# Optimization experiments

Hardware: AMD Instinct MI355X
Metric: run time of the kernel (lower is better)

## Reference

```python
import jax, jax.numpy as jnp
import numpy as np

H = 256      # hidden_dim
NH = 8       # num_heads
D = H // NH  # per-head dim
NEG = -(2.0**32) + 1.0
EPS = 1e-5


def setup_inputs() -> dict:
    key = jax.random.key(0)
    ks = jax.random.split(key, 12)
    N, Tq, Tk = 2, 2048, 2048
    s = 1.0 / np.sqrt(H)
    return {
        "Q": jax.random.normal(ks[0], (N, Tq, H), jnp.float32),
        "K": jax.random.normal(ks[1], (N, Tk, H), jnp.float32),
        "V": jax.random.normal(ks[2], (N, Tk, H), jnp.float32),
        "Wq": jax.random.normal(ks[3], (H, H), jnp.float32) * s,
        "bq": jnp.zeros((H,), jnp.float32),
        "Wk": jax.random.normal(ks[4], (H, H), jnp.float32) * s,
        "bk": jnp.zeros((H,), jnp.float32),
        "Wv": jax.random.normal(ks[5], (H, H), jnp.float32) * s,
        "bv": jnp.zeros((H,), jnp.float32),
        "gamma": jnp.ones((H,), jnp.float32),
        "beta": jnp.zeros((H,), jnp.float32),
    }


def _split_heads(x):
    # [N,T,H] -> [h,N,T,D]  (matches torch split(dim=2)+cat(dim=0): head-major)
    N, T, _ = x.shape
    return x.reshape(N, T, NH, D).transpose(2, 0, 1, 3)


def reference(Q, K, V, Wq, bq, Wk, bk, Wv, bv, gamma, beta):
    N, Tq, _ = Q.shape
    Tk = K.shape[1]
    Ql = jax.nn.relu(Q @ Wq + bq)
    Kl = jax.nn.relu(K @ Wk + bk)
    Vl = jax.nn.relu(V @ Wv + bv)
    Qh, Kh, Vh = _split_heads(Ql), _split_heads(Kl), _split_heads(Vl)

    scores = jnp.einsum("hnqd,hnkd->hnqk", Qh, Kh) / jnp.sqrt(jnp.float32(D))
    key_mask = jnp.sign(jnp.abs(K).sum(-1))    # [N,Tk]
    scores = jnp.where(key_mask[None, :, None, :] == 0, NEG, scores)
    attn = jax.nn.softmax(scores / 0.01, axis=-1)
    query_mask = jnp.sign(jnp.abs(Q).sum(-1))  # [N,Tq]
    attn = attn * query_mask[None, :, :, None]  # dropout p=0 -> identity

    ctx = jnp.einsum("hnqk,hnkd->hnqd", attn[..., :-1], Vh[:, :, :-1, :])
    out = ctx.transpose(1, 2, 0, 3).reshape(N, Tq, H)

    mu = out.mean(-1, keepdims=True)
    var = ((out - mu) ** 2).mean(-1, keepdims=True)
    out = (out - mu) / jnp.sqrt(var + EPS) * gamma + beta

    weight = attn.transpose(1, 2, 0, 3).reshape(N, Tq, NH * Tk).mean(-1)
    return out, weight
```

## Files before the change

### kernel.cpp

```cpp
#include <hip/hip_runtime.h>
#include <math.h>

#define H_DIM 256
#define NHEAD 8
#define DHEAD 32
#define NB 2
#define TSEQ 2048
#define LN_EPS 1e-5f

#define QK2_SCALE 25.503486f
#define SPLIT 4
#define TILES_PER (TSEQ / 64 / SPLIT)

typedef _Float16 half8 __attribute__((ext_vector_type(8)));
typedef _Float16 half4t __attribute__((ext_vector_type(4)));
typedef _Float16 half2t __attribute__((ext_vector_type(2)));
typedef float f32x4 __attribute__((ext_vector_type(4)));

__device__ __forceinline__ f32x4 mfma16(half8 a, half8 b, f32x4 c) {
  return __builtin_amdgcn_mfma_f32_16x16x32_f16(a, b, c, 0, 0, 0);
}
__device__ __forceinline__ float exp2fast(float x) {
  return __builtin_amdgcn_exp2f(x);
}
__device__ __forceinline__ half2t pkrtz(float a, float b) {
  return __builtin_bit_cast(half2t, __builtin_amdgcn_cvt_pkrtz(a, b));
}

#define GLOAD_LDS(gp, lp)                                            \
  __builtin_amdgcn_global_load_lds(                                  \
      (const __attribute__((address_space(1))) void*)(gp),           \
      (__attribute__((address_space(3))) void*)(lp), 16, 0, 0)

__global__ __launch_bounds__(256, 3) void proj_kernel(
    const float* __restrict__ Q, const float* __restrict__ K, const float* __restrict__ V,
    const float* __restrict__ Wq, const float* __restrict__ Wk, const float* __restrict__ Wv,
    const float* __restrict__ bq, const float* __restrict__ bk, const float* __restrict__ bv,
    half8* __restrict__ Gqhi, half8* __restrict__ Gqlo,
    half8* __restrict__ Gkhi, half8* __restrict__ Gklo, half8* __restrict__ Gv,
    float* __restrict__ qmask, float* __restrict__ kmask) {
  const int which = blockIdx.z;
  const float* X    = which == 0 ? Q  : which == 1 ? K  : V;
  const float* Wsel = which == 0 ? Wq : which == 1 ? Wk : Wv;
  const float* bias = which == 0 ? bq : which == 1 ? bk : bv;

  __shared__ __align__(16) float T[64 * 68];

  const int tid = threadIdx.x;
  const int w = tid >> 6, lane = tid & 63;
  const int l15 = lane & 15, quad = lane >> 4;
  const int mbase = blockIdx.y * 64;
  const int nfg   = blockIdx.x * 4;
  const int nn   = mbase >> 11;
  const int tile = blockIdx.y & 31;

  half8 ahi[8], alo[8];
  {
    const bool domask = (blockIdx.x == 0) && (which < 2);
    float sabs = 0.0f;
    const float* xrow = X + (size_t)(mbase + w * 16 + l15) * H_DIM + quad * 8;
    #pragma unroll
    for (int s = 0; s < 8; ++s) {
      float4 a0 = *(const float4*)(xrow + s * 32);
      float4 a1 = *(const float4*)(xrow + s * 32 + 4);
      float xs[8] = {a0.x, a0.y, a0.z, a0.w, a1.x, a1.y, a1.z, a1.w};
      if (domask) {
        #pragma unroll
        for (int i = 0; i < 8; ++i) sabs += fabsf(xs[i]);
      }
      #pragma unroll
      for (int i = 0; i < 8; ++i) {
        _Float16 h = (_Float16)xs[i];
        ahi[s][i] = h;
        alo[s][i] = (_Float16)(xs[i] - (float)h);
      }
    }
    if (domask) {
      sabs += __shfl_xor(sabs, 16);
      sabs += __shfl_xor(sabs, 32);
      float* dst = (which == 0) ? qmask : kmask;
      if (quad == 0) dst[mbase + w * 16 + l15] = (sabs != 0.0f) ? 1.0f : 0.0f;
    }
  }

  f32x4 acc[4];
  #pragma unroll
  for (int f = 0; f < 4; ++f) acc[f] = (f32x4){0.f, 0.f, 0.f, 0.f};

  #pragma unroll
  for (int s = 0; s < 8; ++s) {
    #pragma unroll
    for (int f = 0; f < 4; ++f) {
      const float* wp = Wsel + (size_t)(s * 32 + quad * 8) * H_DIM + (nfg + f) * 16 + l15;
      half8 BH, BL;
      #pragma unroll
      for (int jj = 0; jj < 8; ++jj) {
        float x = wp[(size_t)jj * H_DIM];
        _Float16 h = (_Float16)x;
        BH[jj] = h;
        BL[jj] = (_Float16)(x - (float)h);
      }
      acc[f] = mfma16(ahi[s], BH, acc[f]);
      acc[f] = mfma16(ahi[s], BL, acc[f]);
      acc[f] = mfma16(alo[s], BH, acc[f]);
    }
  }

  #pragma unroll
  for (int f = 0; f < 4; ++f) {
    float bj = bias[blockIdx.x * 64 + f * 16 + l15];
    #pragma unroll
    for (int r = 0; r < 4; ++r) {
      int row = w * 16 + quad * 4 + r;
      float val = fmaxf(acc[f][r] + bj, 0.0f);
      if (which == 2 && ((mbase + row) & (TSEQ - 1)) == TSEQ - 1) val = 0.0f;
      T[row * 68 + f * 16 + l15] = val;
    }
  }
  __syncthreads();

  if (which < 2) {
    const int fq = tid >> 6, lp = tid & 63;
    const int kdc = lp >> 4, krlo = lp & 15;
    const int row = fq * 16 + krlo;
    const float sc = (which == 0) ? QK2_SCALE : 1.0f;
    #pragma unroll
    for (int hs = 0; hs < 2; ++hs) {
      const float* p = &T[row * 68 + hs * 32 + kdc * 8];
      float4 a0 = *(const float4*)p;
      float4 a1 = *(const float4*)(p + 4);
      float xs[8] = {a0.x, a0.y, a0.z, a0.w, a1.x, a1.y, a1.z, a1.w};
      half8 hi, lo;
      #pragma unroll
      for (int i = 0; i < 8; ++i) {
        float x = xs[i] * sc;
        _Float16 h = (_Float16)x;
        hi[i] = h;
        lo[i] = (_Float16)(x - (float)h);
      }
      int hn = (blockIdx.x * 2 + hs) * NB + nn;
      size_t di = ((size_t)hn * 32 + tile) * 256 + tid;
      if (which == 0) { Gqhi[di] = hi; Gqlo[di] = lo; }
      else            { Gkhi[di] = hi; Gklo[di] = lo; }
    }
  } else {
    const int top = tid >> 6, mid = (tid >> 4) & 3, low = tid & 15;
    const int c = top >> 1, hh = top & 1;
    const int trow0 = (c * 4 + mid) * 8;
    #pragma unroll
    for (int hs = 0; hs < 2; ++hs) {
      const int col = hs * 32 + hh * 16 + low;
      half8 v8;
      #pragma unroll
      for (int j = 0; j < 8; ++j)
        v8[j] = (_Float16)T[(trow0 + j) * 68 + col];
      int hn = (blockIdx.x * 2 + hs) * NB + nn;
      Gv[((size_t)hn * 32 + tile) * 256 + tid] = v8;
    }
  }
}

__global__ __launch_bounds__(256, 4) void attn_kernel(
    const half8* __restrict__ Gqhi, const half8* __restrict__ Gqlo,
    const half8* __restrict__ Gkhi, const half8* __restrict__ Gklo,
    const half8* __restrict__ Gv, const float* __restrict__ kmask,
    _Float16* __restrict__ Opf, float* __restrict__ Mp, float* __restrict__ Lp) {
  __shared__ __align__(16) half8 KhB[2][256];
  __shared__ __align__(16) half8 KlB[2][256];
  __shared__ __align__(16) half8 VB[2][256];
  __shared__ __align__(16) float kmS[2][64];
  __shared__ __align__(16) _Float16 Pbuf[4][16][72];

  const int tid = threadIdx.x;
  const int w = tid >> 6, lane = tid & 63;
  const int l15 = lane & 15, quad = lane >> 4;

  const int b = blockIdx.x;
  const int g    = ((b & 7) << 1) | ((b >> 3) & 1);
  const int qt   = (b >> 4) & 15;
  const int sblk = b >> 8;
  const int n = g & 1;

  const size_t fbase = (size_t)g * 32 * 256;
  const int tile0 = sblk * TILES_PER;

  const size_t qoff = fbase + (size_t)(qt * 2) * 256 + w * 64 + lane;
  half8 qhiA = Gqhi[qoff];
  half8 qloA = Gqlo[qoff];
  half8 qhiB = Gqhi[qoff + 256];
  half8 qloB = Gqlo[qoff + 256];

  half8 amONE;
  #pragma unroll
  for (int j = 0; j < 8; ++j) amONE[j] = (l15 == 0) ? (_Float16)1.0f : (_Float16)0.0f;

  float mA = -1.0e30f, mB = -1.0e30f;
  f32x4 O0A = {0.f,0.f,0.f,0.f}, O1A = O0A, OlA = O0A;
  f32x4 O0B = O0A, O1B = O0A, OlB = O0A;

  const half8* gkh = Gkhi + fbase + (size_t)tile0 * 256;
  const half8* gkl = Gklo + fbase + (size_t)tile0 * 256;
  const half8* gvv = Gv   + fbase + (size_t)tile0 * 256;
  const float* kmg = kmask + (size_t)n * TSEQ + tile0 * 64;

  GLOAD_LDS(gkh + tid, &KhB[0][tid]);
  GLOAD_LDS(gkl + tid, &KlB[0][tid]);
  GLOAD_LDS(gvv + tid, &VB[0][tid]);
  if (tid < 16) GLOAD_LDS(kmg + tid * 4, &kmS[0][tid * 4]);
  __syncthreads();

  #pragma unroll
  for (int tt = 0; tt < TILES_PER; ++tt) {
    const int cur = tt & 1, nxt = cur ^ 1;
    if (tt < TILES_PER - 1) {
      GLOAD_LDS(gkh + (tt + 1) * 256 + tid, &KhB[nxt][tid]);
      GLOAD_LDS(gkl + (tt + 1) * 256 + tid, &KlB[nxt][tid]);
      GLOAD_LDS(gvv + (tt + 1) * 256 + tid, &VB[nxt][tid]);
      if (tid < 16) GLOAD_LDS(kmg + (tt + 1) * 64 + tid * 4, &kmS[nxt][tid * 4]);
    }

    f32x4 SA[4], SB[4];
    #pragma unroll
    for (int f = 0; f < 4; ++f) {
      half8 KH = KhB[cur][f * 64 + lane];
      half8 KL = KlB[cur][f * 64 + lane];
      f32x4 a = (f32x4){0.f, 0.f, 0.f, 0.f};
      a = mfma16(KL, qhiA, a);
      a = mfma16(KH, qloA, a);
      a = mfma16(KH, qhiA, a);
      SA[f] = a;
      f32x4 bb = (f32x4){0.f, 0.f, 0.f, 0.f};
      bb = mfma16(KL, qhiB, bb);
      bb = mfma16(KH, qloB, bb);
      bb = mfma16(KH, qhiB, bb);
      SB[f] = bb;
    }

    const half8* vbuf = (const half8*)VB[cur];
    const float* kmP = &kmS[cur][0];

#define SM_PV(S, m_q, O0, O1, Ol)                                              \
    {                                                                          \
      float t0 = fmaxf(fmaxf(S[0][0], S[0][1]), fmaxf(S[0][2], S[0][3]));      \
      float t1 = fmaxf(fmaxf(S[1][0], S[1][1]), fmaxf(S[1][2], S[1][3]));      \
      float t2 = fmaxf(fmaxf(S[2][0], S[2][1]), fmaxf(S[2][2], S[2][3]));      \
      float t3 = fmaxf(fmaxf(S[3][0], S[3][1]), fmaxf(S[3][2], S[3][3]));      \
      float mx = fmaxf(fmaxf(t0, t1), fmaxf(t2, t3));                          \
      mx = fmaxf(mx, __shfl_xor(mx, 16));                                      \
      mx = fmaxf(mx, __shfl_xor(mx, 32));                                      \
      float mnew = fmaxf(m_q, mx);                                             \
      float alpha = exp2fast(m_q - mnew);                                      \
      m_q = mnew;                                                              \
      _Pragma("unroll")                                                        \
      for (int f = 0; f < 4; ++f) {                                            \
        f32x4 kmv = *(const f32x4*)&kmP[f * 16 + quad * 4];                    \
        float p0 = exp2fast(S[f][0] - m_q) * kmv[0];                           \
        float p1 = exp2fast(S[f][1] - m_q) * kmv[1];                           \
        float p2 = exp2fast(S[f][2] - m_q) * kmv[2];                           \
        float p3 = exp2fast(S[f][3] - m_q) * kmv[3];                           \
        half2t a01 = pkrtz(p0, p1);                                            \
        half2t a23 = pkrtz(p2, p3);                                            \
        half4t pk4;                                                            \
        pk4[0] = a01[0]; pk4[1] = a01[1]; pk4[2] = a23[0]; pk4[3] = a23[1];    \
        *(half4t*)&Pbuf[w][l15][f * 16 + quad * 4] = pk4;                      \
      }                                                                        \
      _Pragma("unroll")                                                        \
      for (int r = 0; r < 4; ++r) { O0[r] *= alpha; O1[r] *= alpha; }          \
      Ol[0] *= alpha;                                                          \
      asm volatile("s_waitcnt lgkmcnt(0)" ::: "memory");                       \
      _Pragma("unroll")                                                        \
      for (int c = 0; c < 2; ++c) {                                            \
        half8 pb = *(const half8*)&Pbuf[w][l15][c * 32 + quad * 8];            \
        O0 = mfma16(vbuf[(c * 2 + 0) * 64 + lane], pb, O0);                    \
        O1 = mfma16(vbuf[(c * 2 + 1) * 64 + lane], pb, O1);                    \
        Ol = mfma16(amONE, pb, Ol);                                            \
      }                                                                        \
    }

    SM_PV(SA, mA, O0A, O1A, OlA)
    SM_PV(SB, mB, O0B, O1B, OlB)
#undef SM_PV

    __syncthreads();
  }

  {
    int qA = qt * 128 + w * 16 + l15;
    size_t rowbase = (size_t)(sblk * 16 + g) * TSEQ;
    size_t idxA = (rowbase + qA) * DHEAD;
    size_t idxB = (rowbase + qA + 64) * DHEAD;
    half4t o0A = {(_Float16)O0A[0], (_Float16)O0A[1], (_Float16)O0A[2], (_Float16)O0A[3]};
    half4t o1A = {(_Float16)O1A[0], (_Float16)O1A[1], (_Float16)O1A[2], (_Float16)O1A[3]};
    half4t o0B = {(_Float16)O0B[0], (_Float16)O0B[1], (_Float16)O0B[2], (_Float16)O0B[3]};
    half4t o1B = {(_Float16)O1B[0], (_Float16)O1B[1], (_Float16)O1B[2], (_Float16)O1B[3]};
    *(half4t*)&Opf[idxA + quad * 4]      = o0A;
    *(half4t*)&Opf[idxA + 16 + quad * 4] = o1A;
    *(half4t*)&Opf[idxB + quad * 4]      = o0B;
    *(half4t*)&Opf[idxB + 16 + quad * 4] = o1B;
    if (quad == 0) {
      Mp[rowbase + qA]      = mA;
      Lp[rowbase + qA]      = OlA[0];
      Mp[rowbase + qA + 64] = mB;
      Lp[rowbase + qA + 64] = OlB[0];
    }
  }
}

__global__ __launch_bounds__(256) void ln_kernel(
    const _Float16* __restrict__ Opf, const float* __restrict__ Mp, const float* __restrict__ Lp,
    const float* __restrict__ gamma, const float* __restrict__ beta,
    const float* __restrict__ qmask,
    float* __restrict__ out, float* __restrict__ wout) {
  const int wid = threadIdx.x >> 6, lane = threadIdx.x & 63;
  const int row = blockIdx.x * 4 + wid;
  const int n = row >> 11, q = row & (TSEQ - 1);
  const int hh = lane >> 3;
  const int hn = hh * NB + n;
  const int dbase = (lane & 7) * 4;

  float m[SPLIT], l[SPLIT];
  half4t P[SPLIT];
  #pragma unroll
  for (int i = 0; i < SPLIT; ++i) {
    size_t si = (size_t)(i * 16 + hn) * TSEQ + q;
    P[i] = *(const half4t*)&Opf[si * DHEAD + dbase];
    m[i] = Mp[si];
    l[i] = Lp[si];
  }
  float mm = m[0];
  #pragma unroll
  for (int i = 1; i < SPLIT; ++i) mm = fmaxf(mm, m[i]);
  float denom = 0.f;
  float a[SPLIT];
  #pragma unroll
  for (int i = 0; i < SPLIT; ++i) { a[i] = exp2fast(m[i] - mm); denom += l[i] * a[i]; }
  float qm = qmask[row];
  float inv = qm / denom;

  float4 x = make_float4(0.f, 0.f, 0.f, 0.f);
  #pragma unroll
  for (int i = 0; i < SPLIT; ++i) {
    x.x += (float)P[i][0] * a[i]; x.y += (float)P[i][1] * a[i];
    x.z += (float)P[i][2] * a[i]; x.w += (float)P[i][3] * a[i];
  }
  x.x *= inv; x.y *= inv; x.z *= inv; x.w *= inv;

  float s = x.x + x.y + x.z + x.w;
  #pragma unroll
  for (int off = 32; off > 0; off >>= 1) s += __shfl_xor(s, off);
  float mu = s * (1.0f / H_DIM);
  float dx0 = x.x - mu, dx1 = x.y - mu, dx2 = x.z - mu, dx3 = x.w - mu;
  float sq = dx0 * dx0 + dx1 * dx1 + dx2 * dx2 + dx3 * dx3;
  #pragma unroll
  for (int off = 32; off > 0; off >>= 1) sq += __shfl_xor(sq, off);
  float rstd = rsqrtf(sq * (1.0f / H_DIM) + LN_EPS);
  float4 g = *(const float4*)(gamma + lane * 4);
  float4 bb = *(const float4*)(beta + lane * 4);
  float4 y;
  y.x = dx0 * rstd * g.x + bb.x;
  y.y = dx1 * rstd * g.y + bb.y;
  y.z = dx2 * rstd * g.z + bb.z;
  y.w = dx3 * rstd * g.w + bb.w;
  *(float4*)(out + (size_t)row * H_DIM + lane * 4) = y;
  if (lane == 0) wout[row] = qm * (1.0f / TSEQ);
}

extern "C" void kernel_launch(void* const* d_in, const int* in_sizes, int n_in,
                              void* d_out, int out_size, void* d_ws, size_t ws_size,
                              hipStream_t stream) {
  const float* Q  = (const float*)d_in[0];
  const float* K  = (const float*)d_in[1];
  const float* V  = (const float*)d_in[2];
  const float* Wq = (const float*)d_in[3];
  const float* bq = (const float*)d_in[4];
  const float* Wk = (const float*)d_in[5];
  const float* bk = (const float*)d_in[6];
  const float* Wv = (const float*)d_in[7];
  const float* bv = (const float*)d_in[8];
  const float* gamma = (const float*)d_in[9];
  const float* beta  = (const float*)d_in[10];

  char* ws = (char*)d_ws;
  const size_t NFRAG = (size_t)16 * 32 * 256;
  _Float16* Opf = (_Float16*)ws;
  half8* Gqhi = (half8*)(ws + (size_t)SPLIT * 16 * TSEQ * DHEAD * 2);
  half8* Gqlo = Gqhi + NFRAG;
  half8* Gkhi = Gqlo + NFRAG;
  half8* Gklo = Gkhi + NFRAG;
  half8* Gv   = Gklo + NFRAG;
  float* Mp = (float*)(Gv + NFRAG);
  float* Lp = Mp + SPLIT * 16 * TSEQ;
  float* qmask = Lp + SPLIT * 16 * TSEQ;
  float* kmask = qmask + NB * TSEQ;

  float* out  = (float*)d_out;
  float* wout = out + (size_t)NB * TSEQ * H_DIM;

  hipLaunchKernelGGL(proj_kernel, dim3(H_DIM / 64, NB * TSEQ / 64, 3), dim3(256), 0, stream,
                     Q, K, V, Wq, Wk, Wv, bq, bk, bv,
                     Gqhi, Gqlo, Gkhi, Gklo, Gv, qmask, kmask);
  hipLaunchKernelGGL(attn_kernel, dim3(16 * 16 * SPLIT), dim3(256), 0, stream,
                     Gqhi, Gqlo, Gkhi, Gklo, Gv, kmask, Opf, Mp, Lp);
  hipLaunchKernelGGL(ln_kernel, dim3(NB * TSEQ / 4), dim3(256), 0, stream,
                     Opf, Mp, Lp, gamma, beta, qmask, out, wout);
}
```

Baseline: 126.6 us.

## Pre-pack split-fp16 weights once and narrow projection tiles to one head

Adds a pre-pass kernel that computes the key mask and converts Wq/Wk/Wv once into hi/lo fp16 fragments laid out in MFMA order. The projection kernel then loads these packed fragments directly instead of re-reading strided fp32 weights and re-splitting them in every block. Each block now covers one 32-wide head instead of 64 columns, which doubles the grid and halves the accumulators and shared memory, so occupancy can rise. The cost is an extra kernel launch, extra workspace, and each input row being loaded twice as often.

Result: slower. 132.9 us (+5.0%).

```diff
diff --git a/kernel.cpp b/kernel.cpp
--- a/kernel.cpp
+++ b/kernel.cpp
@@ -32,31 +32,67 @@
       (const __attribute__((address_space(1))) void*)(gp),           \
       (__attribute__((address_space(3))) void*)(lp), 16, 0, 0)
 
-__global__ __launch_bounds__(256, 3) void proj_kernel(
+__global__ __launch_bounds__(256) void pack_mask_kernel(
+    const float* __restrict__ K,
+    const float* __restrict__ Wq, const float* __restrict__ Wk, const float* __restrict__ Wv,
+    float* __restrict__ kmask,
+    half8* __restrict__ WpkHi, half8* __restrict__ WpkLo) {
+  const int tid = threadIdx.x;
+  if (blockIdx.x < 1024) {
+    const int wid = tid >> 6, lane = tid & 63;
+    int row = blockIdx.x * 4 + wid;
+    const float* src = K + (size_t)row * H_DIM;
+    float4 v = *(const float4*)(src + lane * 4);
+    float s = fabsf(v.x) + fabsf(v.y) + fabsf(v.z) + fabsf(v.w);
+    #pragma unroll
+    for (int off = 32; off > 0; off >>= 1) s += __shfl_xor(s, off);
+    if (lane == 0) kmask[row] = (s != 0.0f) ? 1.0f : 0.0f;
+    return;
+  }
+  int slot = (blockIdx.x - 1024) * 256 + tid;
+  int lane = slot & 63;
+  int fg = (slot >> 6) & 15;
+  int s  = (slot >> 10) & 7;
+  int which = slot >> 13;
+  const float* W = which == 0 ? Wq : which == 1 ? Wk : Wv;
+  int j  = fg * 16 + (lane & 15);
+  int kb = s * 32 + (lane >> 4) * 8;
+  half8 hi, lo;
+  #pragma unroll
+  for (int jj = 0; jj < 8; ++jj) {
+    float x = W[(size_t)(kb + jj) * H_DIM + j];
+    _Float16 h = (_Float16)x;
+    hi[jj] = h;
+    lo[jj] = (_Float16)(x - (float)h);
+  }
+  WpkHi[slot] = hi;
+  WpkLo[slot] = lo;
+}
+
+__global__ __launch_bounds__(256, 4) void proj_kernel(
     const float* __restrict__ Q, const float* __restrict__ K, const float* __restrict__ V,
-    const float* __restrict__ Wq, const float* __restrict__ Wk, const float* __restrict__ Wv,
     const float* __restrict__ bq, const float* __restrict__ bk, const float* __restrict__ bv,
+    const half8* __restrict__ WpkHi, const half8* __restrict__ WpkLo,
     half8* __restrict__ Gqhi, half8* __restrict__ Gqlo,
     half8* __restrict__ Gkhi, half8* __restrict__ Gklo, half8* __restrict__ Gv,
-    float* __restrict__ qmask, float* __restrict__ kmask) {
+    float* __restrict__ qmask) {
   const int which = blockIdx.z;
   const float* X    = which == 0 ? Q  : which == 1 ? K  : V;
-  const float* Wsel = which == 0 ? Wq : which == 1 ? Wk : Wv;
   const float* bias = which == 0 ? bq : which == 1 ? bk : bv;
 
-  __shared__ __align__(16) float T[64 * 68];
+  __shared__ __align__(16) float T[64 * 36];
 
   const int tid = threadIdx.x;
   const int w = tid >> 6, lane = tid & 63;
   const int l15 = lane & 15, quad = lane >> 4;
   const int mbase = blockIdx.y * 64;
-  const int nfg   = blockIdx.x * 4;
+  const int xh    = blockIdx.x;
   const int nn   = mbase >> 11;
   const int tile = blockIdx.y & 31;
 
   half8 ahi[8], alo[8];
   {
-    const bool domask = (blockIdx.x == 0) && (which < 2);
+    const bool doqm = (which == 0) && (xh == 0);
     float sabs = 0.0f;
     const float* xrow = X + (size_t)(mbase + w * 16 + l15) * H_DIM + quad * 8;
     #pragma unroll
@@ -64,7 +100,7 @@
       float4 a0 = *(const float4*)(xrow + s * 32);
       float4 a1 = *(const float4*)(xrow + s * 32 + 4);
       float xs[8] = {a0.x, a0.y, a0.z, a0.w, a1.x, a1.y, a1.z, a1.w};
-      if (domask) {
+      if (doqm) {
         #pragma unroll
         for (int i = 0; i < 8; ++i) sabs += fabsf(xs[i]);
       }
@@ -75,31 +111,25 @@
         alo[s][i] = (_Float16)(xs[i] - (float)h);
       }
     }
-    if (domask) {
+    if (doqm) {
       sabs += __shfl_xor(sabs, 16);
       sabs += __shfl_xor(sabs, 32);
-      float* dst = (which == 0) ? qmask : kmask;
-      if (quad == 0) dst[mbase + w * 16 + l15] = (sabs != 0.0f) ? 1.0f : 0.0f;
-    }
-  }
-
-  f32x4 acc[4];
-  #pragma unroll
-  for (int f = 0; f < 4; ++f) acc[f] = (f32x4){0.f, 0.f, 0.f, 0.f};
+      if (quad == 0) qmask[mbase + w * 16 + l15] = (sabs != 0.0f) ? 1.0f : 0.0f;
+    }
+  }
+
+  f32x4 acc[2];
+  #pragma unroll
+  for (int f = 0; f < 2; ++f) acc[f] = (f32x4){0.f, 0.f, 0.f, 0.f};
 
   #pragma unroll
   for (int s = 0; s < 8; ++s) {
-    #pragma unroll
-    for (int f = 0; f < 4; ++f) {
-      const float* wp = Wsel + (size_t)(s * 32 + quad * 8) * H_DIM + (nfg + f) * 16 + l15;
-      half8 BH, BL;
-      #pragma unroll
-      for (int jj = 0; jj < 8; ++jj) {
-        float x = wp[(size_t)jj * H_DIM];
-        _Float16 h = (_Float16)x;
-        BH[jj] = h;
-        BL[jj] = (_Float16)(x - (float)h);
-      }
+    const half8* ph = WpkHi + (((size_t)which * 8 + s) * 16 + xh * 2) * 64 + lane;
+    const half8* pl = WpkLo + (((size_t)which * 8 + s) * 16 + xh * 2) * 64 + lane;
+    #pragma unroll
+    for (int f = 0; f < 2; ++f) {
+      half8 BH = ph[f * 64];
+      half8 BL = pl[f * 64];
       acc[f] = mfma16(ahi[s], BH, acc[f]);
       acc[f] = mfma16(ahi[s], BL, acc[f]);
       acc[f] = mfma16(alo[s], BH, acc[f]);
@@ -107,56 +137,49 @@
   }
 
   #pragma unroll
-  for (int f = 0; f < 4; ++f) {
-    float bj = bias[blockIdx.x * 64 + f * 16 + l15];
+  for (int f = 0; f < 2; ++f) {
+    float bj = bias[xh * 32 + f * 16 + l15];
     #pragma unroll
     for (int r = 0; r < 4; ++r) {
       int row = w * 16 + quad * 4 + r;
       float val = fmaxf(acc[f][r] + bj, 0.0f);
       if (which == 2 && ((mbase + row) & (TSEQ - 1)) == TSEQ - 1) val = 0.0f;
-      T[row * 68 + f * 16 + l15] = val;
+      T[row * 36 + f * 16 + l15] = val;
     }
   }
   __syncthreads();
 
+  const int hn = xh * NB + nn;
   if (which < 2) {
     const int fq = tid >> 6, lp = tid & 63;
     const int kdc = lp >> 4, krlo = lp & 15;
     const int row = fq * 16 + krlo;
     const float sc = (which == 0) ? QK2_SCALE : 1.0f;
-    #pragma unroll
-    for (int hs = 0; hs < 2; ++hs) {
-      const float* p = &T[row * 68 + hs * 32 + kdc * 8];
-      float4 a0 = *(const float4*)p;
-      float4 a1 = *(const float4*)(p + 4);
-      float xs[8] = {a0.x, a0.y, a0.z, a0.w, a1.x, a1.y, a1.z, a1.w};
-      half8 hi, lo;
-      #pragma unroll
-      for (int i = 0; i < 8; ++i) {
-        float x = xs[i] * sc;
-        _Float16 h = (_Float16)x;
-        hi[i] = h;
-        lo[i] = (_Float16)(x - (float)h);
-      }
-      int hn = (blockIdx.x * 2 + hs) * NB + nn;
-      size_t di = ((size_t)hn * 32 + tile) * 256 + tid;
-      if (which == 0) { Gqhi[di] = hi; Gqlo[di] = lo; }
-      else            { Gkhi[di] = hi; Gklo[di] = lo; }
-    }
+    const float* p = &T[row * 36 + kdc * 8];
+    float4 a0 = *(const float4*)p;
+    float4 a1 = *(const float4*)(p + 4);
+    float xs[8] = {a0.x, a0.y, a0.z, a0.w, a1.x, a1.y, a1.z, a1.w};
+    half8 hi, lo;
+    #pragma unroll
+    for (int i = 0; i < 8; ++i) {
+      float x = xs[i] * sc;
+      _Float16 h = (_Float16)x;
+      hi[i] = h;
+      lo[i] = (_Float16)(x - (float)h);
+    }
+    size_t di = ((size_t)hn * 32 + tile) * 256 + tid;
+    if (which == 0) { Gqhi[di] = hi; Gqlo[di] = lo; }
+    else            { Gkhi[di] = hi; Gklo[di] = lo; }
   } else {
     const int top = tid >> 6, mid = (tid >> 4) & 3, low = tid & 15;
     const int c = top >> 1, hh = top & 1;
     const int trow0 = (c * 4 + mid) * 8;
-    #pragma unroll
-    for (int hs = 0; hs < 2; ++hs) {
-      const int col = hs * 32 + hh * 16 + low;
-      half8 v8;
-      #pragma unroll
-      for (int j = 0; j < 8; ++j)
-        v8[j] = (_Float16)T[(trow0 + j) * 68 + col];
-      int hn = (blockIdx.x * 2 + hs) * NB + nn;
-      Gv[((size_t)hn * 32 + tile) * 256 + tid] = v8;
-    }
+    const int col = hh * 16 + low;
+    half8 v8;
+    #pragma unroll
+    for (int j = 0; j < 8; ++j)
+      v8[j] = (_Float16)T[(trow0 + j) * 36 + col];
+    Gv[((size_t)hn * 32 + tile) * 256 + tid] = v8;
   }
 }
 
@@ -392,13 +415,17 @@
   float* Lp = Mp + SPLIT * 16 * TSEQ;
   float* qmask = Lp + SPLIT * 16 * TSEQ;
   float* kmask = qmask + NB * TSEQ;
+  half8* WpkHi = (half8*)(kmask + NB * TSEQ);
+  half8* WpkLo = WpkHi + 24576;
 
   float* out  = (float*)d_out;
   float* wout = out + (size_t)NB * TSEQ * H_DIM;
 
-  hipLaunchKernelGGL(proj_kernel, dim3(H_DIM / 64, NB * TSEQ / 64, 3), dim3(256), 0, stream,
-                     Q, K, V, Wq, Wk, Wv, bq, bk, bv,
-                     Gqhi, Gqlo, Gkhi, Gklo, Gv, qmask, kmask);
+  hipLaunchKernelGGL(pack_mask_kernel, dim3(1024 + 96), dim3(256), 0, stream,
+                     K, Wq, Wk, Wv, kmask, WpkHi, WpkLo);
+  hipLaunchKernelGGL(proj_kernel, dim3(8, NB * TSEQ / 64, 3), dim3(256), 0, stream,
+                     Q, K, V, bq, bk, bv, WpkHi, WpkLo,
+                     Gqhi, Gqlo, Gkhi, Gklo, Gv, qmask);
   hipLaunchKernelGGL(attn_kernel, dim3(16 * 16 * SPLIT), dim3(256), 0, stream,
                      Gqhi, Gqlo, Gkhi, Gklo, Gv, kmask, Opf, Mp, Lp);
   hipLaunchKernelGGL(ln_kernel, dim3(NB * TSEQ / 4), dim3(256), 0, stream,
```
